# Kernel optimization log

Hardware: AMD Instinct MI355X
Metric: run time of the kernel (lower is better)

Reference implementation:

```python
import jax, jax.numpy as jnp
import numpy as np

B, NB, D, H = 16384, 3, 1024, 8
HD = D // H
EPS = 1e-5

def setup_inputs() -> dict:
    key = jax.random.key(0)
    ks = jax.random.split(key, 24)
    w = lambda k, shp: jax.random.normal(k, shp, jnp.float32) * 0.02
    return {
        "x": jax.random.normal(ks[0], (B, NB, D), jnp.float32),
        # nn.MultiheadAttention params
        "in_proj_w": w(ks[1], (3 * D, D)),
        "in_proj_b": jnp.zeros((3 * D,), jnp.float32),
        "out_w": w(ks[2], (D, D)),
        "out_b": jnp.zeros((D,), jnp.float32),
        # weight_generator MLP
        "wg1_w": w(ks[3], (D, D * NB)), "wg1_b": jnp.zeros((D,), jnp.float32),
        "wg2_w": w(ks[4], (D // 2, D)), "wg2_b": jnp.zeros((D // 2,), jnp.float32),
        "wg3_w": w(ks[5], (NB, D // 2)), "wg3_b": jnp.zeros((NB,), jnp.float32),
        # refiner MLP + LayerNorms
        "r1_w": w(ks[6], (2 * D, D)), "r1_b": jnp.zeros((2 * D,), jnp.float32),
        "ln1_g": jnp.ones((2 * D,), jnp.float32), "ln1_b": jnp.zeros((2 * D,), jnp.float32),
        "r2_w": w(ks[7], (D, 2 * D)), "r2_b": jnp.zeros((D,), jnp.float32),
        "ln2_g": jnp.ones((D,), jnp.float32), "ln2_b": jnp.zeros((D,), jnp.float32),
    }

def _layernorm(x, g, b):
    m = jnp.mean(x, axis=-1, keepdims=True)
    v = jnp.mean(jnp.square(x - m), axis=-1, keepdims=True)
    return (x - m) * jax.lax.rsqrt(v + EPS) * g + b

def _forward(x, in_proj_w, in_proj_b, out_w, out_b,
             wg1_w, wg1_b, wg2_w, wg2_b, wg3_w, wg3_b,
             r1_w, r1_b, ln1_g, ln1_b, r2_w, r2_b, ln2_g, ln2_b):
    b = x.shape[0]
    # --- cross (self) attention over the NB branch tokens ---
    qkv = jnp.einsum("bsd,ed->bse", x, in_proj_w) + in_proj_b  # [B, NB, 3D]
    q, k, v = jnp.split(qkv, 3, axis=-1)
    q = q.reshape(b, NB, H, HD)
    k = k.reshape(b, NB, H, HD)
    v = v.reshape(b, NB, H, HD)
    scores = jnp.einsum("bqhd,bkhd->bhqk", q, k) / jnp.sqrt(jnp.float32(HD))
    attn = jax.nn.softmax(scores, axis=-1)
    o = jnp.einsum("bhqk,bkhd->bqhd", attn, v).reshape(b, NB, D)
    attended = jnp.einsum("bsd,ed->bse", o, out_w) + out_b  # [B, NB, D]
    # --- dynamic softmax gate over branches ---
    flat = attended.reshape(b, NB * D)
    h = jax.nn.relu(flat @ wg1_w.T + wg1_b)
    h = jax.nn.relu(h @ wg2_w.T + wg2_b)
    weights = jax.nn.softmax(h @ wg3_w.T + wg3_b, axis=-1)  # [B, NB]
    weighted = jnp.einsum("bsd,bs->bd", attended, weights)  # [B, D]
    # --- refiner (dropout inactive in eval) ---
    h = weighted @ r1_w.T + r1_b
    h = jax.nn.relu(_layernorm(h, ln1_g, ln1_b))
    out = h @ r2_w.T + r2_b
    return _layernorm(out, ln2_g, ln2_b)

def reference(x, in_proj_w, in_proj_b, out_w, out_b,
              wg1_w, wg1_b, wg2_w, wg2_b, wg3_w, wg3_b,
              r1_w, r1_b, ln1_g, ln1_b, r2_w, r2_b, ln2_g, ln2_b):
    return _forward(x, in_proj_w, in_proj_b, out_w, out_b,
                    wg1_w, wg1_b, wg2_w, wg2_b, wg3_w, wg3_b,
                    r1_w, r1_b, ln1_g, ln1_b, r2_w, r2_b, ln2_g, ln2_b)
```

## Files before the change

### kernel.cpp

```cpp
#include <hip/hip_runtime.h>
#include <hip/hip_bf16.h>

#define BB   16384
#define NBR  3
#define DD   1024
#define HH   8
#define HDD  128

typedef __attribute__((ext_vector_type(8))) short short8;
typedef __attribute__((ext_vector_type(4))) float f32x4;

__device__ __forceinline__ float b2f(ushort u) {
    union { unsigned int i; float f; } x; x.i = ((unsigned int)u) << 16; return x.f;
}
__device__ __forceinline__ ushort f2b(float f) {
    union { __hip_bfloat16 h; ushort u; } x; x.h = __float2bfloat16(f); return x.u;
}

__global__ __launch_bounds__(256) void cvt_f32_bf16(const float* __restrict__ in,
                                                    ushort* __restrict__ out, long n) {
    long i = ((long)blockIdx.x * 256 + threadIdx.x) * 4;
    if (i + 4 > n) return;
    float4 v = *reinterpret_cast<const float4*>(in + i);
    unsigned int a = ((unsigned int)f2b(v.x)) | (((unsigned int)f2b(v.y)) << 16);
    unsigned int b = ((unsigned int)f2b(v.z)) | (((unsigned int)f2b(v.w)) << 16);
    uint2 p; p.x = a; p.y = b;
    *reinterpret_cast<uint2*>(out + i) = p;
}

__global__ __launch_bounds__(256) void transpose_cvt(const float* __restrict__ in,
                                                     ushort* __restrict__ out) {
    __shared__ float t[32][33];
    const int bx = blockIdx.x & 31, by = blockIdx.x >> 5;
    const int tx = threadIdx.x & 31, ty = threadIdx.x >> 5;
    #pragma unroll
    for (int i = 0; i < 4; i++)
        t[ty + i * 8][tx] = in[(size_t)(by * 32 + ty + i * 8) * 1024 + bx * 32 + tx];
    __syncthreads();
    #pragma unroll
    for (int i = 0; i < 4; i++)
        out[(size_t)(bx * 32 + ty + i * 8) * 1024 + by * 32 + tx] = f2b(t[tx][ty + i * 8]);
}

__global__ __launch_bounds__(256) void bias1_kernel(const float* __restrict__ wg1w,
                                                    const float* __restrict__ wg1b,
                                                    const float* __restrict__ outb,
                                                    float* __restrict__ b1p) {
    const int o = (blockIdx.x * 256 + threadIdx.x) >> 6;
    const int lane = threadIdx.x & 63;
    const float* wr = wg1w + (size_t)o * 3072;
    float s = 0.f;
    for (int e = lane; e < 1024; e += 64)
        s += outb[e] * (wr[e] + wr[e + 1024] + wr[e + 2048]);
    #pragma unroll
    for (int off = 32; off; off >>= 1) s += __shfl_xor(s, off, 64);
    if (lane == 0) b1p[o] = s + wg1b[o];
}

template<int EPI>
__global__ __launch_bounds__(512, 2)
void gemm256(const ushort* __restrict__ A, const ushort* __restrict__ Bt,
             const float* __restrict__ bias, void* __restrict__ Cout,
             int M, int N, int K) {
    extern __shared__ ushort lds[];

    const int tid  = threadIdx.x;
    const int wid  = tid >> 6;
    const int lane = tid & 63;
    const int cpx  = gridDim.x >> 3;
    const int bid  = (blockIdx.x & 7) * cpx + (blockIdx.x >> 3);
    const int nbn  = N >> 8;
    const int bm   = bid / nbn;
    const int bn   = bid % nbn;
    const long m0  = (long)bm * 256;
    const long n0  = (long)bn * 256;
    const int NT   = K >> 6;

    const int srow = tid >> 3;
    const int kel  = (((tid & 7) ^ (srow & 7)) << 3);
    const int widEl = wid * 512;

    const ushort* gA[2][2];
    const ushort* gB[2][2];
    #pragma unroll
    for (int c = 0; c < 2; c++)
        #pragma unroll
        for (int j = 0; j < 2; j++) {
            gA[c][j] = A  + (size_t)(m0 + c * 128 + j * 64 + srow) * K + kel;
            gB[c][j] = Bt + (size_t)(n0 + c * 128 + j * 64 + srow) * K + kel;
        }

    const int wr = wid >> 2, wc = wid & 3;
    const int lm15 = lane & 15;
    int aoff[8];
    #pragma unroll
    for (int m = 0; m < 8; m++) aoff[m] = (wr * 128 + m * 16 + lm15) * 64;
    int boff[4];
    #pragma unroll
    for (int c = 0; c < 4; c++) boff[c] = (wc * 64 + c * 16 + lm15) * 64;
    const int kbr[2] = {
        (((0 << 6) | ((lane >> 4) << 4)) ^ ((lane & 7) << 4)) >> 1,
        (((1 << 6) | ((lane >> 4) << 4)) ^ ((lane & 7) << 4)) >> 1
    };

    f32x4 acc[8][4];
    #pragma unroll
    for (int m = 0; m < 8; m++)
        #pragma unroll
        for (int c = 0; c < 4; c++) { f32x4 z = {0.f, 0.f, 0.f, 0.f}; acc[m][c] = z; }

    short8 af[8], bf[2];

#define STAGE(C, PB, TT) { \
    const ushort* _g0; const ushort* _g1; int _b; \
    if ((C) < 2) { _g0 = gA[(C)][0] + (TT) * 64; _g1 = gA[(C)][1] + (TT) * 64; \
                   _b = (PB) * 16384 + (C) * 8192 + widEl; } \
    else         { _g0 = gB[(C) - 2][0] + (TT) * 64; _g1 = gB[(C) - 2][1] + (TT) * 64; \
                   _b = 32768 + (PB) * 16384 + ((C) - 2) * 8192 + widEl; } \
    __builtin_amdgcn_global_load_lds((const __attribute__((address_space(1))) void*)_g0, \
        (__attribute__((address_space(3))) void*)&lds[_b], 16, 0, 0); \
    __builtin_amdgcn_global_load_lds((const __attribute__((address_space(1))) void*)_g1, \
        (__attribute__((address_space(3))) void*)&lds[_b + 4096], 16, 0, 0); }

#define READ_A(P, KK) { \
    _Pragma("unroll") \
    for (int _m = 0; _m < 8; _m++) \
        af[_m] = *(const short8*)&lds[(P) * 16384 + aoff[_m] + kbr[KK]]; }

#define READ_B2(P, KK, C0) { \
    bf[0] = *(const short8*)&lds[32768 + (P) * 16384 + boff[(C0)] + kbr[KK]]; \
    bf[1] = *(const short8*)&lds[32768 + (P) * 16384 + boff[(C0) + 1] + kbr[KK]]; }

#define MFMA8x2(C0) { \
    _Pragma("unroll") \
    for (int _m = 0; _m < 8; _m++) { \
        acc[_m][(C0)]     = __builtin_amdgcn_mfma_f32_16x16x32_bf16(af[_m], bf[0], acc[_m][(C0)], 0, 0, 0); \
        acc[_m][(C0) + 1] = __builtin_amdgcn_mfma_f32_16x16x32_bf16(af[_m], bf[1], acc[_m][(C0) + 1], 0, 0, 0); } }

#define TILE_STEP(P, T, PRE) { \
     \
    if (PRE) STAGE(0, (P) ^ 1, (T) + 1); \
    if (PRE) { asm volatile("s_waitcnt vmcnt(2)" ::: "memory"); } \
    else     { asm volatile("s_waitcnt vmcnt(0)" ::: "memory"); } \
    __builtin_amdgcn_s_barrier(); \
    asm volatile("" ::: "memory"); \
    __builtin_amdgcn_sched_barrier(0); \
    READ_A(P, 0); \
    READ_B2(P, 0, 0); \
    __builtin_amdgcn_s_setprio(1); MFMA8x2(0); __builtin_amdgcn_s_setprio(0); \
    __builtin_amdgcn_s_barrier(); \
     \
    if (PRE) STAGE(1, (P) ^ 1, (T) + 1); \
    READ_B2(P, 0, 2); \
    __builtin_amdgcn_s_barrier(); \
    __builtin_amdgcn_s_setprio(1); MFMA8x2(2); __builtin_amdgcn_s_setprio(0); \
    __builtin_amdgcn_s_barrier(); \
     \
    if (PRE) STAGE(2, (P) ^ 1, (T) + 1); \
    READ_A(P, 1); \
    READ_B2(P, 1, 0); \
    __builtin_amdgcn_s_barrier(); \
    __builtin_amdgcn_s_setprio(1); MFMA8x2(0); __builtin_amdgcn_s_setprio(0); \
    __builtin_amdgcn_s_barrier(); \
     \
    if (PRE) STAGE(3, (P) ^ 1, (T) + 1); \
    READ_B2(P, 1, 2); \
    __builtin_amdgcn_s_barrier(); \
    __builtin_amdgcn_s_setprio(1); MFMA8x2(2); __builtin_amdgcn_s_setprio(0); \
    __builtin_amdgcn_s_barrier(); }

    STAGE(0, 0, 0); STAGE(1, 0, 0); STAGE(2, 0, 0); STAGE(3, 0, 0);

    int t = 0;
    for (; t + 2 < NT; t += 2) {
        TILE_STEP(0, t, true);
        TILE_STEP(1, t + 1, true);
    }
    TILE_STEP(0, t, true);
    TILE_STEP(1, t + 1, false);

#undef TILE_STEP
#undef MFMA8x2
#undef READ_B2
#undef READ_A
#undef STAGE

    const int l16 = lane >> 4;
    #pragma unroll
    for (int c = 0; c < 4; c++) {
        const long col = n0 + wc * 64 + c * 16 + lm15;
        const float bc = bias[col];
        #pragma unroll
        for (int m = 0; m < 8; m++) {
            const long row = m0 + wr * 128 + m * 16 + l16 * 4;
            #pragma unroll
            for (int j = 0; j < 4; j++) {
                float v = acc[m][c][j] + bc;
                if (EPI == 1) v = v > 0.f ? v : 0.f;
                if (EPI == 2) ((float*)Cout)[(row + j) * (long)N + col] = v;
                else          ((ushort*)Cout)[(row + j) * (long)N + col] = f2b(v);
            }
        }
    }
}

template<int EPI>
__global__ __launch_bounds__(256, 2)
void gemm_bt(const ushort* __restrict__ A, const ushort* __restrict__ Bt,
             const float* __restrict__ bias, void* __restrict__ Cout,
             int M, int N, int K, int lda, int ldb, int ldc, int sA, int sC) {
    __shared__ ushort As[128 * 64];
    __shared__ ushort Bs[128 * 64];
    const int tid  = threadIdx.x;
    const int wid  = tid >> 6;
    const int lane = tid & 63;
    const int cpx  = gridDim.x >> 3;
    const int bid  = (blockIdx.x & 7) * cpx + (blockIdx.x >> 3);
    const int nbn  = N >> 7;
    const int bm   = bid / nbn;
    const int bn   = bid % nbn;
    const long m0  = (long)bm * 128;
    const long n0  = (long)bn * 128;

    A += (size_t)blockIdx.y * sA;
    const long cOff = (long)blockIdx.y * sC;

    const int srow = tid >> 3;
    const int scol = (tid & 7) << 3;
    const ushort* gA = A  + (m0 + srow) * (long)lda + scol;
    const ushort* gB = Bt + (n0 + srow) * (long)ldb + scol;

    f32x4 acc[4][4];
    #pragma unroll
    for (int i = 0; i < 4; i++)
        #pragma unroll
        for (int j = 0; j < 4; j++) { f32x4 z = {0.f, 0.f, 0.f, 0.f}; acc[i][j] = z; }

    const int wr = wid >> 1, wc = wid & 1;
    const int kits = K >> 6;

    for (int kt = 0; kt < kits; ++kt) {
        const ushort* pA = gA + kt * 64;
        const ushort* pB = gB + kt * 64;
        #pragma unroll
        for (int i = 0; i < 4; i++) {
            __builtin_amdgcn_global_load_lds(
                (const __attribute__((address_space(1))) void*)(pA + (long)i * 32 * lda),
                (__attribute__((address_space(3))) void*)&As[(i * 32 + wid * 8) * 64],
                16, 0, 0);
        }
        #pragma unroll
        for (int i = 0; i < 4; i++) {
            __builtin_amdgcn_global_load_lds(
                (const __attribute__((address_space(1))) void*)(pB + (long)i * 32 * ldb),
                (__attribute__((address_space(3))) void*)&Bs[(i * 32 + wid * 8) * 64],
                16, 0, 0);
        }
        __syncthreads();
        #pragma unroll
        for (int kk = 0; kk < 2; kk++) {
            const int ko = kk * 32 + (lane >> 4) * 8;
            short8 af[4], bf[4];
            #pragma unroll
            for (int m = 0; m < 4; m++)
                af[m] = *(const short8*)&As[(wr * 64 + m * 16 + (lane & 15)) * 64 + ko];
            #pragma unroll
            for (int n = 0; n < 4; n++)
                bf[n] = *(const short8*)&Bs[(wc * 64 + n * 16 + (lane & 15)) * 64 + ko];
            #pragma unroll
            for (int m = 0; m < 4; m++)
                #pragma unroll
                for (int n = 0; n < 4; n++)
                    acc[m][n] = __builtin_amdgcn_mfma_f32_16x16x32_bf16(af[m], bf[n], acc[m][n], 0, 0, 0);
        }
        __syncthreads();
    }

    #pragma unroll
    for (int n = 0; n < 4; n++) {
        const long c = n0 + wc * 64 + n * 16 + (lane & 15);
        const float bc = bias[c];
        #pragma unroll
        for (int m = 0; m < 4; m++) {
            const long r = m0 + wr * 64 + m * 16 + (lane >> 4) * 4;
            #pragma unroll
            for (int j = 0; j < 4; j++) {
                float v = acc[m][n][j] + bc;
                if (EPI == 1) v = v > 0.f ? v : 0.f;
                if (EPI == 2) ((float*)Cout)[(r + j) * (long)ldc + cOff + c] = v;
                else          ((ushort*)Cout)[(r + j) * (long)ldc + cOff + c] = f2b(v);
            }
        }
    }
}

__global__ __launch_bounds__(256) void attn_kernel(const ushort* __restrict__ qkv,
                                                   ushort* __restrict__ o) {
    const int w    = (blockIdx.x * 256 + threadIdx.x) >> 6;
    const int lane = threadIdx.x & 63;
    const int b = w >> 3, h = w & 7;
    const ushort* base = qkv + (size_t)b * (3 * 3072) + h * HDD + lane * 2;

    float q[3][2], k[3][2], v[3][2];
    #pragma unroll
    for (int i = 0; i < 3; i++) {
        unsigned int qu = *(const unsigned int*)(base + i * 3072);
        unsigned int ku = *(const unsigned int*)(base + i * 3072 + 1024);
        unsigned int vu = *(const unsigned int*)(base + i * 3072 + 2048);
        q[i][0] = b2f((ushort)(qu & 0xffff)); q[i][1] = b2f((ushort)(qu >> 16));
        k[i][0] = b2f((ushort)(ku & 0xffff)); k[i][1] = b2f((ushort)(ku >> 16));
        v[i][0] = b2f((ushort)(vu & 0xffff)); v[i][1] = b2f((ushort)(vu >> 16));
    }

    float s[3][3];
    #pragma unroll
    for (int i = 0; i < 3; i++)
        #pragma unroll
        for (int j = 0; j < 3; j++)
            s[i][j] = q[i][0] * k[j][0] + q[i][1] * k[j][1];

    #pragma unroll
    for (int off = 32; off; off >>= 1)
        #pragma unroll
        for (int i = 0; i < 3; i++)
            #pragma unroll
            for (int j = 0; j < 3; j++)
                s[i][j] += __shfl_xor(s[i][j], off, 64);

    const float sc = 0.08838834764831845f;
    float a[3][3];
    #pragma unroll
    for (int i = 0; i < 3; i++) {
        float l0 = s[i][0] * sc, l1 = s[i][1] * sc, l2 = s[i][2] * sc;
        float mx = fmaxf(fmaxf(l0, l1), l2);
        float e0 = __expf(l0 - mx), e1 = __expf(l1 - mx), e2 = __expf(l2 - mx);
        float inv = 1.f / (e0 + e1 + e2);
        a[i][0] = e0 * inv; a[i][1] = e1 * inv; a[i][2] = e2 * inv;
    }

    ushort* ob = o + (size_t)b * 3072 + h * HDD + lane * 2;
    #pragma unroll
    for (int i = 0; i < 3; i++) {
        float o0 = a[i][0] * v[0][0] + a[i][1] * v[1][0] + a[i][2] * v[2][0];
        float o1 = a[i][0] * v[0][1] + a[i][1] * v[1][1] + a[i][2] * v[2][1];
        unsigned int pk = ((unsigned int)f2b(o0)) | (((unsigned int)f2b(o1)) << 16);
        *(unsigned int*)(ob + i * 1024) = pk;
    }
}

__global__ __launch_bounds__(256) void gate_kernel(const ushort* __restrict__ h2,
                                                   const float* __restrict__ w3,
                                                   const float* __restrict__ b3,
                                                   const ushort* __restrict__ att,
                                                   ushort* __restrict__ weighted) {
    const int gw = (blockIdx.x * 256 + threadIdx.x) >> 6;
    const int lane = threadIdx.x & 63;
    if (gw >= BB) return;

    const ushort* hr = h2 + (size_t)gw * 512 + lane * 8;
    short8 hv = *(const short8*)hr;
    float hf[8];
    #pragma unroll
    for (int d = 0; d < 8; d++) hf[d] = b2f((ushort)hv[d]);

    float dot[3];
    #pragma unroll
    for (int s = 0; s < 3; s++) {
        const float* wr = w3 + s * 512 + lane * 8;
        float4 wa = *(const float4*)wr;
        float4 wb = *(const float4*)(wr + 4);
        dot[s] = hf[0] * wa.x + hf[1] * wa.y + hf[2] * wa.z + hf[3] * wa.w
               + hf[4] * wb.x + hf[5] * wb.y + hf[6] * wb.z + hf[7] * wb.w;
    }
    #pragma unroll
    for (int off = 32; off; off >>= 1)
        #pragma unroll
        for (int s = 0; s < 3; s++) dot[s] += __shfl_xor(dot[s], off, 64);

    float l0 = dot[0] + b3[0], l1 = dot[1] + b3[1], l2 = dot[2] + b3[2];
    float mx = fmaxf(fmaxf(l0, l1), l2);
    float e0 = __expf(l0 - mx), e1 = __expf(l1 - mx), e2 = __expf(l2 - mx);
    float inv = 1.f / (e0 + e1 + e2);
    float w0 = e0 * inv, w1 = e1 * inv, w2 = e2 * inv;

    const ushort* ab = att + (size_t)gw * 3072;
    ushort* wb = weighted + (size_t)gw * 1024;
    #pragma unroll
    for (int i = 0; i < 2; i++) {
        int d0 = (i * 64 + lane) * 8;
        short8 a0 = *(const short8*)(ab + d0);
        short8 a1 = *(const short8*)(ab + 1024 + d0);
        short8 a2 = *(const short8*)(ab + 2048 + d0);
        short8 r;
        #pragma unroll
        for (int d = 0; d < 8; d++) {
            float v = w0 * b2f((ushort)a0[d]) + w1 * b2f((ushort)a1[d]) + w2 * b2f((ushort)a2[d]);
            r[d] = (short)f2b(v);
        }
        *(short8*)(wb + d0) = r;
    }
}

template<int W, int RELU, int OUTBF16>
__global__ __launch_bounds__(256) void ln_kernel(const ushort* __restrict__ in,
                                                 const float* __restrict__ g,
                                                 const float* __restrict__ bt,
                                                 void* __restrict__ out) {
    constexpr int E = W / 256;
    const int row = blockIdx.x;
    const ushort* xr = in + (size_t)row * W + threadIdx.x * E;

    float v[E];
    if (E == 8) {
        uint4 raw = *reinterpret_cast<const uint4*>(xr);
        const unsigned int* rw = (const unsigned int*)&raw;
        #pragma unroll
        for (int p = 0; p < 4; p++) {
            v[2 * p]     = b2f((ushort)(rw[p] & 0xffff));
            v[2 * p + 1] = b2f((ushort)(rw[p] >> 16));
        }
    } else {
        uint2 raw = *reinterpret_cast<const uint2*>(xr);
        const unsigned int* rw = (const unsigned int*)&raw;
        #pragma unroll
        for (int p = 0; p < 2; p++) {
            v[2 * p]     = b2f((ushort)(rw[p] & 0xffff));
            v[2 * p + 1] = b2f((ushort)(rw[p] >> 16));
        }
    }

    float s = 0.f;
    #pragma unroll
    for (int e = 0; e < E; e++) s += v[e];

    __shared__ float red1[4], red2[4];
    const int wid = threadIdx.x >> 6, lane = threadIdx.x & 63;
    #pragma unroll
    for (int off = 32; off; off >>= 1) s += __shfl_xor(s, off, 64);
    if (lane == 0) red1[wid] = s;
    __syncthreads();
    const float mean = (red1[0] + red1[1] + red1[2] + red1[3]) / (float)W;

    float q = 0.f;
    #pragma unroll
    for (int e = 0; e < E; e++) { float d = v[e] - mean; q += d * d; }
    #pragma unroll
    for (int off = 32; off; off >>= 1) q += __shfl_xor(q, off, 64);
    if (lane == 0) red2[wid] = q;
    __syncthreads();
    const float var = (red2[0] + red2[1] + red2[2] + red2[3]) / (float)W;
    const float rstd = rsqrtf(var + 1e-5f);

    const int c0 = threadIdx.x * E;
    float o[E];
    #pragma unroll
    for (int e = 0; e < E; e++) {
        float ov = (v[e] - mean) * rstd * g[c0 + e] + bt[c0 + e];
        if (RELU) ov = ov > 0.f ? ov : 0.f;
        o[e] = ov;
    }
    if (OUTBF16) {
        ushort* op = (ushort*)out + (size_t)row * W + c0;
        unsigned int pk[E / 2];
        #pragma unroll
        for (int p = 0; p < E / 2; p++)
            pk[p] = ((unsigned int)f2b(o[2 * p])) | (((unsigned int)f2b(o[2 * p + 1])) << 16);
        if (E == 8) *reinterpret_cast<uint4*>(op) = *(uint4*)pk;
        else        *reinterpret_cast<uint2*>(op) = *(uint2*)pk;
    } else {
        float* op = (float*)out + (size_t)row * W + c0;
        #pragma unroll
        for (int p = 0; p < E / 4; p++)
            reinterpret_cast<float4*>(op)[p] = ((float4*)o)[p];
    }
}

extern "C" void kernel_launch(void* const* d_in, const int* in_sizes, int n_in,
                              void* d_out, int out_size, void* d_ws, size_t ws_size,
                              hipStream_t stream) {
    const float* x    = (const float*)d_in[0];
    const float* ipw  = (const float*)d_in[1];
    const float* ipb  = (const float*)d_in[2];
    const float* outw = (const float*)d_in[3];
    const float* outb = (const float*)d_in[4];
    const float* wg1w = (const float*)d_in[5];
    const float* wg1b = (const float*)d_in[6];
    const float* wg2w = (const float*)d_in[7];
    const float* wg2b = (const float*)d_in[8];
    const float* wg3w = (const float*)d_in[9];
    const float* wg3b = (const float*)d_in[10];
    const float* r1w  = (const float*)d_in[11];
    const float* r1b  = (const float*)d_in[12];
    const float* ln1g = (const float*)d_in[13];
    const float* ln1b = (const float*)d_in[14];
    const float* r2w  = (const float*)d_in[15];
    const float* r2b  = (const float*)d_in[16];
    const float* ln2g = (const float*)d_in[17];
    const float* ln2b = (const float*)d_in[18];

    char* ws = (char*)d_ws;
    ushort* w_ip  = (ushort*)(ws + 0);
    ushort* w_out = (ushort*)(ws + 6291456);
    ushort* w_g1  = (ushort*)(ws + 8388608);
    ushort* w_g2  = (ushort*)(ws + 14680064);
    ushort* w_r1  = (ushort*)(ws + 15728640);
    ushort* w_r2  = (ushort*)(ws + 19922944);
    char* R1 = ws + 24117248;
    char* R2 = ws + 124780544;

    ushort* xb       = (ushort*)R1;
    ushort* qkv      = (ushort*)R2;
    ushort* o_att    = (ushort*)R1;
    ushort* h1       = (ushort*)(R2 + 0);
    ushort* h2       = (ushort*)(R2 + 33554432);
    ushort* wsum_o   = (ushort*)(R2 + 50331648);
    ushort* weighted = (ushort*)(R2 + 83886080);
    ushort* r1out    = (ushort*)(R2 + 117440512);
    ushort* r2out    = (ushort*)(R2 + 184549376);
    ushort* w1p      = (ushort*)(R2 + 218103808);
    ushort* w_outT   = (ushort*)(R2 + 224395264);
    float*  b1p      = (float*) (R2 + 226492416);
    float*  zbias    = (float*) (R2 + 226496512);
    ushort* ln1out   = (ushort*)R1;

    (void)hipFuncSetAttribute((const void*)gemm256<0>, hipFuncAttributeMaxDynamicSharedMemorySize, 131072);
    (void)hipFuncSetAttribute((const void*)gemm256<1>, hipFuncAttributeMaxDynamicSharedMemorySize, 131072);
    (void)hipFuncSetAttribute((const void*)gemm256<2>, hipFuncAttributeMaxDynamicSharedMemorySize, 131072);

    cvt_f32_bf16<<<49152, 256, 0, stream>>>(x,    xb,   (long)49152 * 1024);
    cvt_f32_bf16<<<3072,  256, 0, stream>>>(ipw,  w_ip, (long)3072 * 1024);
    cvt_f32_bf16<<<1024,  256, 0, stream>>>(outw, w_out,(long)1024 * 1024);
    cvt_f32_bf16<<<3072,  256, 0, stream>>>(wg1w, w_g1, (long)1024 * 3072);
    cvt_f32_bf16<<<512,   256, 0, stream>>>(wg2w, w_g2, (long)512 * 1024);
    cvt_f32_bf16<<<2048,  256, 0, stream>>>(r1w,  w_r1, (long)2048 * 1024);
    cvt_f32_bf16<<<2048,  256, 0, stream>>>(r2w,  w_r2, (long)1024 * 2048);

    gemm256<0><<<192 * 12, 512, 131072, stream>>>(xb, w_ip, ipb, qkv, 49152, 3072, 1024);
    attn_kernel<<<32768, 256, 0, stream>>>(qkv, o_att);

    (void)hipMemsetAsync(zbias, 0, 4096, stream);
    transpose_cvt<<<1024, 256, 0, stream>>>(outw, w_outT);
    gemm_bt<0><<<dim3(64, 3), 256, 0, stream>>>(w_g1, w_outT, zbias, w1p,
                                                1024, 1024, 1024, 3072, 1024, 3072, 1024, 1024);
    bias1_kernel<<<256, 256, 0, stream>>>(wg1w, wg1b, outb, b1p);

    gemm256<1><<<64 * 4, 512, 131072, stream>>>(o_att, w1p, b1p, h1, 16384, 1024, 3072);
    gemm_bt<1><<<dim3(128 * 4, 1), 256, 0, stream>>>(h1, w_g2, wg2b, h2,
                                                     16384, 512, 1024, 1024, 1024, 512, 0, 0);
    gate_kernel<<<4096, 256, 0, stream>>>(h2, wg3w, wg3b, o_att, wsum_o);

    gemm256<0><<<64 * 4, 512, 131072, stream>>>(wsum_o, w_out, outb, weighted, 16384, 1024, 1024);

    gemm256<0><<<64 * 8, 512, 131072, stream>>>(weighted, w_r1, r1b, r1out, 16384, 2048, 1024);
    ln_kernel<2048, 1, 1><<<16384, 256, 0, stream>>>(r1out, ln1g, ln1b, ln1out);
    gemm256<0><<<64 * 4, 512, 131072, stream>>>(ln1out, w_r2, r2b, r2out, 16384, 1024, 2048);
    ln_kernel<1024, 0, 0><<<16384, 256, 0, stream>>>(r2out, ln2g, ln2b, d_out);
}
```

Baseline: 885.9 us.

## Fold out_proj into refiner first layer weights and vectorize GEMM epilogue stores

Precomputes r1_w·out_w as a combined weight (plus folded bias), so the gated sum of attention outputs goes straight into the refiner's first GEMM. This drops the separate 16384x1024x1024 out-projection GEMM and its intermediate buffer. It also swaps the MFMA operand order in gemm256 so each lane holds four consecutive columns, letting the epilogue do a float4 bias load and packed 8-byte bf16 stores. The cost is a small weight-only GEMM and bias-fold kernel per call, plus an extra bf16 rounding of the combined weights.

```diff
diff --git a/kernel.cpp b/kernel.cpp
--- a/kernel.cpp
+++ b/kernel.cpp
@@ -55,6 +55,20 @@
     #pragma unroll
     for (int off = 32; off; off >>= 1) s += __shfl_xor(s, off, 64);
     if (lane == 0) b1p[o] = s + wg1b[o];
+}
+
+__global__ __launch_bounds__(256) void biasfold_kernel(const float* __restrict__ w,
+                                                       const float* __restrict__ bin,
+                                                       const float* __restrict__ badd,
+                                                       float* __restrict__ outb, int K) {
+    const int o = (blockIdx.x * 256 + threadIdx.x) >> 6;
+    const int lane = threadIdx.x & 63;
+    const float* wr = w + (size_t)o * K;
+    float s = 0.f;
+    for (int e = lane; e < K; e += 64) s += bin[e] * wr[e];
+    #pragma unroll
+    for (int off = 32; off; off >>= 1) s += __shfl_xor(s, off, 64);
+    if (lane == 0) outb[o] = s + badd[o];
 }
 
 template<int EPI>
@@ -134,8 +148,8 @@
 #define MFMA8x2(C0) { \
     _Pragma("unroll") \
     for (int _m = 0; _m < 8; _m++) { \
-        acc[_m][(C0)]     = __builtin_amdgcn_mfma_f32_16x16x32_bf16(af[_m], bf[0], acc[_m][(C0)], 0, 0, 0); \
-        acc[_m][(C0) + 1] = __builtin_amdgcn_mfma_f32_16x16x32_bf16(af[_m], bf[1], acc[_m][(C0) + 1], 0, 0, 0); } }
+        acc[_m][(C0)]     = __builtin_amdgcn_mfma_f32_16x16x32_bf16(bf[0], af[_m], acc[_m][(C0)], 0, 0, 0); \
+        acc[_m][(C0) + 1] = __builtin_amdgcn_mfma_f32_16x16x32_bf16(bf[1], af[_m], acc[_m][(C0) + 1], 0, 0, 0); } }
 
 #define TILE_STEP(P, T, PRE) { \
      \
@@ -188,18 +202,23 @@
     const int l16 = lane >> 4;
     #pragma unroll
     for (int c = 0; c < 4; c++) {
-        const long col = n0 + wc * 64 + c * 16 + lm15;
-        const float bc = bias[col];
+        const long colb = n0 + wc * 64 + c * 16 + l16 * 4;
+        const float4 b4 = *(const float4*)&bias[colb];
         #pragma unroll
         for (int m = 0; m < 8; m++) {
-            const long row = m0 + wr * 128 + m * 16 + l16 * 4;
-            #pragma unroll
-            for (int j = 0; j < 4; j++) {
-                float v = acc[m][c][j] + bc;
-                if (EPI == 1) v = v > 0.f ? v : 0.f;
-                if (EPI == 2) ((float*)Cout)[(row + j) * (long)N + col] = v;
-                else          ((ushort*)Cout)[(row + j) * (long)N + col] = f2b(v);
+            const long row = m0 + wr * 128 + m * 16 + lm15;
+            float v0 = acc[m][c][0] + b4.x;
+            float v1 = acc[m][c][1] + b4.y;
+            float v2 = acc[m][c][2] + b4.z;
+            float v3 = acc[m][c][3] + b4.w;
+            if (EPI == 1) {
+                v0 = v0 > 0.f ? v0 : 0.f; v1 = v1 > 0.f ? v1 : 0.f;
+                v2 = v2 > 0.f ? v2 : 0.f; v3 = v3 > 0.f ? v3 : 0.f;
             }
+            uint2 st;
+            st.x = ((unsigned int)f2b(v0)) | (((unsigned int)f2b(v1)) << 16);
+            st.y = ((unsigned int)f2b(v2)) | (((unsigned int)f2b(v3)) << 16);
+            *reinterpret_cast<uint2*>(&((ushort*)Cout)[row * (long)N + colb]) = st;
         }
     }
 }
@@ -287,8 +306,7 @@
             for (int j = 0; j < 4; j++) {
                 float v = acc[m][n][j] + bc;
                 if (EPI == 1) v = v > 0.f ? v : 0.f;
-                if (EPI == 2) ((float*)Cout)[(r + j) * (long)ldc + cOff + c] = v;
-                else          ((ushort*)Cout)[(r + j) * (long)ldc + cOff + c] = f2b(v);
+                ((ushort*)Cout)[(r + j) * (long)ldc + cOff + c] = f2b(v);
             }
         }
     }
@@ -514,22 +532,21 @@
     ushort* h1       = (ushort*)(R2 + 0);
     ushort* h2       = (ushort*)(R2 + 33554432);
     ushort* wsum_o   = (ushort*)(R2 + 50331648);
-    ushort* weighted = (ushort*)(R2 + 83886080);
     ushort* r1out    = (ushort*)(R2 + 117440512);
     ushort* r2out    = (ushort*)(R2 + 184549376);
     ushort* w1p      = (ushort*)(R2 + 218103808);
     ushort* w_outT   = (ushort*)(R2 + 224395264);
     float*  b1p      = (float*) (R2 + 226492416);
     float*  zbias    = (float*) (R2 + 226496512);
+    ushort* w_r1c    = (ushort*)(R2 + 226500608);
+    float*  b_r1c    = (float*) (R2 + 230694912);
     ushort* ln1out   = (ushort*)R1;
 
     (void)hipFuncSetAttribute((const void*)gemm256<0>, hipFuncAttributeMaxDynamicSharedMemorySize, 131072);
     (void)hipFuncSetAttribute((const void*)gemm256<1>, hipFuncAttributeMaxDynamicSharedMemorySize, 131072);
-    (void)hipFuncSetAttribute((const void*)gemm256<2>, hipFuncAttributeMaxDynamicSharedMemorySize, 131072);
 
     cvt_f32_bf16<<<49152, 256, 0, stream>>>(x,    xb,   (long)49152 * 1024);
     cvt_f32_bf16<<<3072,  256, 0, stream>>>(ipw,  w_ip, (long)3072 * 1024);
-    cvt_f32_bf16<<<1024,  256, 0, stream>>>(outw, w_out,(long)1024 * 1024);
     cvt_f32_bf16<<<3072,  256, 0, stream>>>(wg1w, w_g1, (long)1024 * 3072);
     cvt_f32_bf16<<<512,   256, 0, stream>>>(wg2w, w_g2, (long)512 * 1024);
     cvt_f32_bf16<<<2048,  256, 0, stream>>>(r1w,  w_r1, (long)2048 * 1024);
@@ -543,15 +560,16 @@
     gemm_bt<0><<<dim3(64, 3), 256, 0, stream>>>(w_g1, w_outT, zbias, w1p,
                                                 1024, 1024, 1024, 3072, 1024, 3072, 1024, 1024);
     bias1_kernel<<<256, 256, 0, stream>>>(wg1w, wg1b, outb, b1p);
+    gemm_bt<0><<<dim3(128, 1), 256, 0, stream>>>(w_r1, w_outT, zbias, w_r1c,
+                                                 2048, 1024, 1024, 1024, 1024, 1024, 0, 0);
+    biasfold_kernel<<<512, 256, 0, stream>>>(r1w, outb, r1b, b_r1c, 1024);
 
     gemm256<1><<<64 * 4, 512, 131072, stream>>>(o_att, w1p, b1p, h1, 16384, 1024, 3072);
     gemm_bt<1><<<dim3(128 * 4, 1), 256, 0, stream>>>(h1, w_g2, wg2b, h2,
                                                      16384, 512, 1024, 1024, 1024, 512, 0, 0);
     gate_kernel<<<4096, 256, 0, stream>>>(h2, wg3w, wg3b, o_att, wsum_o);
 
-    gemm256<0><<<64 * 4, 512, 131072, stream>>>(wsum_o, w_out, outb, weighted, 16384, 1024, 1024);
-
-    gemm256<0><<<64 * 8, 512, 131072, stream>>>(weighted, w_r1, r1b, r1out, 16384, 2048, 1024);
+    gemm256<0><<<64 * 8, 512, 131072, stream>>>(wsum_o, w_r1c, b_r1c, r1out, 16384, 2048, 1024);
     ln_kernel<2048, 1, 1><<<16384, 256, 0, stream>>>(r1out, ln1g, ln1b, ln1out);
     gemm256<0><<<64 * 4, 512, 131072, stream>>>(ln1out, w_r2, r2b, r2out, 16384, 1024, 2048);
     ln_kernel<1024, 0, 0><<<16384, 256, 0, stream>>>(r2out, ln2g, ln2b, d_out);
```

Result: no change. 893.8 us (+0.9%).
